# Kernel optimization log

Hardware: AMD Instinct MI355X
Metric: run time of the kernel (lower is better)

The kernel has to match this reference:

```python
import jax, jax.numpy as jnp
import numpy as np
import math

N_HEAD = 8
LN_EPS = 1e-5


def _layernorm(x, w, b):
    # Biased variance as in the triton kernel: var = E[x^2] - mean^2
    mean = jnp.mean(x, axis=-1, keepdims=True)
    var = jnp.mean(x * x, axis=-1, keepdims=True) - mean * mean
    return (x - mean) * jax.lax.rsqrt(var + LN_EPS) * w + b


def _gelu_tanh(x):
    # matches triton gelu: tanh approximation
    return 0.5 * x * (1.0 + jnp.tanh(0.7978845608 * (x + 0.044715 * x * x * x)))


def _causal_attention(qkv, n_head):
    B, T, C3 = qkv.shape
    C = C3 // 3
    D = C // n_head
    q, k, v = jnp.split(qkv, 3, axis=-1)
    q = q.reshape(B, T, n_head, D)
    k = k.reshape(B, T, n_head, D)
    v = v.reshape(B, T, n_head, D)
    scale = 1.0 / math.sqrt(D)
    scores = jnp.einsum('bqhd,bkhd->bhqk', q, k) * scale  # [B,H,T,T]
    causal = jnp.tril(jnp.ones((T, T), dtype=bool))
    scores = jnp.where(causal, scores, -jnp.inf)
    p = jax.nn.softmax(scores, axis=-1)
    out = jnp.einsum('bhqk,bkhd->bqhd', p, v)
    return out.reshape(B, T, C)


def setup_inputs() -> dict:
    key = jax.random.key(0)
    ks = jax.random.split(key, 8)
    B, T, C = 8, 2048, 768
    s = 0.02
    return {
        'x': jax.random.normal(ks[0], (B, T, C), jnp.float32),
        'ln1_w': jnp.ones((C,), jnp.float32),
        'ln1_b': jnp.zeros((C,), jnp.float32),
        'w_qkv': jax.random.normal(ks[1], (3 * C, C), jnp.float32) * s,
        'b_qkv': jnp.zeros((3 * C,), jnp.float32),
        'w_attn_proj': jax.random.normal(ks[2], (C, C), jnp.float32) * s,
        'b_attn_proj': jnp.zeros((C,), jnp.float32),
        'ln2_w': jnp.ones((C,), jnp.float32),
        'ln2_b': jnp.zeros((C,), jnp.float32),
        'w_fc': jax.random.normal(ks[3], (4 * C, C), jnp.float32) * s,
        'b_fc': jnp.zeros((4 * C,), jnp.float32),
        'w_mlp_proj': jax.random.normal(ks[4], (C, 4 * C), jnp.float32) * s,
        'b_mlp_proj': jnp.zeros((C,), jnp.float32),
    }


def reference(x, ln1_w, ln1_b, w_qkv, b_qkv, w_attn_proj, b_attn_proj,
              ln2_w, ln2_b, w_fc, b_fc, w_mlp_proj, b_mlp_proj):
    # attention block: fused LN + QKV linear, causal flash attention, out proj, residual
    qkv = _layernorm(x, ln1_w, ln1_b) @ w_qkv.T + b_qkv          # [B,T,3C]
    att = _causal_attention(qkv, N_HEAD)                          # [B,T,C]
    x = x + (att @ w_attn_proj.T + b_attn_proj)
    # MLP block: fused LN + fc + gelu, proj, residual
    h = _gelu_tanh(_layernorm(x, ln2_w, ln2_b) @ w_fc.T + b_fc)   # [B,T,4C]
    x = x + (h @ w_mlp_proj.T + b_mlp_proj)
    return x
```

## Files before the change

### kernel.cpp

```cpp
#include <hip/hip_runtime.h>
#include <hip/hip_bf16.h>
#include <cstdint>
#include <cstddef>

typedef __attribute__((ext_vector_type(8))) short bf16x8;
typedef __attribute__((ext_vector_type(4))) short bf16x4;
typedef __attribute__((ext_vector_type(4))) float f32x4;
typedef __attribute__((ext_vector_type(16))) float f32x16;

#define GLB_AS(p) ((const __attribute__((address_space(1))) void*)(p))
#define LDS_AS(p) ((__attribute__((address_space(3))) void*)(p))

__device__ __forceinline__ short f2bf(float f) {
    union { float f; unsigned u; } x; x.f = f;
    unsigned r = (x.u + 0x7fffu + ((x.u >> 16) & 1u)) >> 16;
    return (short)r;
}
__device__ __forceinline__ unsigned packbf2(float a, float b) {
    union { float f; unsigned u; } x, y; x.f = a; y.f = b;
    return (x.u >> 16) | (y.u & 0xffff0000u);
}
__device__ __forceinline__ f32x4 MF(bf16x8 a, bf16x8 b, f32x4 c) {
    return __builtin_amdgcn_mfma_f32_16x16x32_bf16(a, b, c, 0, 0, 0);
}
__device__ __forceinline__ f32x16 MF32(bf16x8 a, bf16x8 b, f32x16 c) {
    return __builtin_amdgcn_mfma_f32_32x32x16_bf16(a, b, c, 0, 0, 0);
}

__global__ __launch_bounds__(256) void k_cast_bf16(const float* __restrict__ src,
                                                   short* __restrict__ dst, int n4) {
    int i = blockIdx.x * 256 + threadIdx.x;
    int stride = gridDim.x * 256;
    for (; i < n4; i += stride) {
        float4 v = ((const float4*)src)[i];
        bf16x4 o;
        o[0] = f2bf(v.x); o[1] = f2bf(v.y); o[2] = f2bf(v.z); o[3] = f2bf(v.w);
        ((bf16x4*)dst)[i] = o;
    }
}

__global__ __launch_bounds__(256) void k_layernorm(const float* __restrict__ x,
                                                   const float* __restrict__ w,
                                                   const float* __restrict__ b,
                                                   short* __restrict__ out) {
    const int row = blockIdx.x;
    const int tid = threadIdx.x;
    const float* xr = x + (size_t)row * 768;
    float v0 = xr[tid], v1 = xr[tid + 256], v2 = xr[tid + 512];
    float s = v0 + v1 + v2;
    float ss = v0 * v0 + v1 * v1 + v2 * v2;
    #pragma unroll
    for (int m = 32; m; m >>= 1) { s += __shfl_xor(s, m); ss += __shfl_xor(ss, m); }
    __shared__ float red[8];
    int wid = tid >> 6, lane = tid & 63;
    if (lane == 0) { red[wid] = s; red[4 + wid] = ss; }
    __syncthreads();
    s = red[0] + red[1] + red[2] + red[3];
    ss = red[4] + red[5] + red[6] + red[7];
    float mean = s * (1.f / 768.f);
    float var = ss * (1.f / 768.f) - mean * mean;
    float inv = rsqrtf(var + 1e-5f);
    short* orow = out + (size_t)row * 768;
    orow[tid]       = f2bf((v0 - mean) * inv * w[tid]       + b[tid]);
    orow[tid + 256] = f2bf((v1 - mean) * inv * w[tid + 256] + b[tid + 256]);
    orow[tid + 512] = f2bf((v2 - mean) * inv * w[tid + 512] + b[tid + 512]);
}

#define QUAD(MB, NB, AA, BB)                                                   \
    do {                                                                       \
        __builtin_amdgcn_s_setprio(1);                                         \
        _Pragma("unroll")                                                      \
        for (int mi = 0; mi < 4; ++mi)                                         \
            _Pragma("unroll")                                                  \
            for (int ni = 0; ni < 2; ++ni) {                                   \
                acc[(MB) + mi][(NB) + ni] =                                    \
                    MF(AA[mi][0], BB[ni][0], acc[(MB) + mi][(NB) + ni]);       \
                acc[(MB) + mi][(NB) + ni] =                                    \
                    MF(AA[mi][1], BB[ni][1], acc[(MB) + mi][(NB) + ni]);       \
            }                                                                  \
        __builtin_amdgcn_s_setprio(0);                                         \
    } while (0)

template <int EPI>
__global__ __launch_bounds__(512, 2) void k_gemm256(const short* __restrict__ A,
                                                    const short* __restrict__ B,
                                                    const float* __restrict__ bias,
                                                    const float* __restrict__ res,
                                                    void* __restrict__ out,
                                                    int M, int N, int K) {
    __shared__ short As3[3][256 * 64];
    __shared__ short Bs2[2][256 * 64];
    const int tid = threadIdx.x, lane = tid & 63, wid = tid >> 6;
    const int l4 = lane & 15, lh = lane >> 4;
    const int wm = wid >> 2, wn = wid & 3;
    const int gx = gridDim.x;
    const int nwg = gx * gridDim.y;
    int wg = blockIdx.y * gx + blockIdx.x;
    { const int q = nwg >> 3; wg = (wg & 7) * q + (wg >> 3); }
    const int row0 = (wg / gx) * 256, col0 = (wg % gx) * 256;

    auto stage = [&](const short* __restrict__ src, int base_row, short* lds,
                     int mh, int k0) {
        #pragma unroll
        for (int i = 0; i < 2; ++i) {
            const int chunk = wid * 2 + i;
            const int dl = mh * 16384 + chunk * 1024 + lane * 16;
            const int r = dl >> 7;
            const int cb = (dl & 127) ^ ((r & 7) << 4);
            __builtin_amdgcn_global_load_lds(
                GLB_AS(src + (size_t)(base_row + r) * K + k0 + (cb >> 1)),
                LDS_AS(lds + mh * 8192 + chunk * 512), 16, 0, 0);
        }
    };
    auto rd = [&](const short* lds, int r, int kb) -> bf16x8 {
        return *(const bf16x8*)((const char*)lds + r * 128 +
                                ((kb * 64 + lh * 16) ^ ((r & 7) << 4)));
    };

    f32x4 acc[8][4] = {};
    bf16x8 a[4][2], b0[2][2], b1[2][2];
    const int NT = K >> 6;

    stage(A, row0, As3[0], 0, 0);  stage(A, row0, As3[0], 1, 0);
    stage(B, col0, Bs2[0], 0, 0);  stage(B, col0, Bs2[0], 1, 0);
    stage(A, row0, As3[1], 0, 64); stage(A, row0, As3[1], 1, 64);
    asm volatile("s_waitcnt vmcnt(4)" ::: "memory");
    __builtin_amdgcn_s_barrier();

    int ia = 0, ia2 = 2, ib = 0;
    for (int t = 0; t < NT; ++t) {
        const short* Ac = As3[ia];
        const short* Bc = Bs2[ib];
        const int ib2 = ib ^ 1;
        #pragma unroll
        for (int mi = 0; mi < 4; ++mi) {
            const int r = wm * 128 + mi * 16 + l4;
            a[mi][0] = rd(Ac, r, 0); a[mi][1] = rd(Ac, r, 1);
        }
        #pragma unroll
        for (int ni = 0; ni < 2; ++ni) {
            const int r = wn * 64 + ni * 16 + l4;
            b0[ni][0] = rd(Bc, r, 0); b0[ni][1] = rd(Bc, r, 1);
        }
        if (t + 1 < NT) {
            const int kn = (t + 1) << 6;
            stage(B, col0, Bs2[ib2], 0, kn);
            stage(B, col0, Bs2[ib2], 1, kn);
        }
        if (t + 2 < NT) {
            const int kn2 = (t + 2) << 6;
            stage(A, row0, As3[ia2], 0, kn2);
            stage(A, row0, As3[ia2], 1, kn2);
        }
        QUAD(0, 0, a, b0);
        __builtin_amdgcn_s_barrier();
        #pragma unroll
        for (int ni = 0; ni < 2; ++ni) {
            const int r = wn * 64 + (2 + ni) * 16 + l4;
            b1[ni][0] = rd(Bc, r, 0); b1[ni][1] = rd(Bc, r, 1);
        }
        QUAD(0, 2, a, b1);
        __builtin_amdgcn_s_barrier();
        #pragma unroll
        for (int mi = 0; mi < 4; ++mi) {
            const int r = wm * 128 + (4 + mi) * 16 + l4;
            a[mi][0] = rd(Ac, r, 0); a[mi][1] = rd(Ac, r, 1);
        }
        QUAD(4, 2, a, b1);
        __builtin_amdgcn_s_barrier();
        QUAD(4, 0, a, b0);
        if (t + 2 < NT) {
            asm volatile("s_waitcnt vmcnt(4)" ::: "memory");
        } else if (t + 1 < NT) {
            asm volatile("s_waitcnt vmcnt(0)" ::: "memory");
        }
        __builtin_amdgcn_s_barrier();
        ia = (ia + 1 == 3) ? 0 : ia + 1;
        ia2 = (ia2 + 1 == 3) ? 0 : ia2 + 1;
        ib = ib2;
    }

    #pragma unroll
    for (int mi = 0; mi < 8; ++mi) {
        const int rowb = row0 + wm * 128 + mi * 16 + lh * 4;
        #pragma unroll
        for (int ni = 0; ni < 4; ++ni) {
            const int col = col0 + wn * 64 + ni * 16 + l4;
            const float bv = bias[col];
            #pragma unroll
            for (int j = 0; j < 4; ++j) {
                const size_t idx = (size_t)(rowb + j) * N + col;
                float v = acc[mi][ni][j] + bv;
                if (EPI == 0) {
                    ((short*)out)[idx] = f2bf(v);
                } else if (EPI == 1) {
                    ((float*)out)[idx] = v + res[idx];
                } else {
                    float u = v + 0.044715f * v * v * v;
                    float t = 1.f - 2.f / (__expf(1.5957691216f * u) + 1.f);
                    ((short*)out)[idx] = f2bf(0.5f * v * (1.f + t));
                }
            }
        }
    }
}

__global__ __launch_bounds__(256, 2) void k_attn6(const short* __restrict__ qkv,
                                                  short* __restrict__ att) {
    __shared__ short Ks[2][64 * 128];
    __shared__ short Vs[2][96 * 64];
    const int tid = threadIdx.x, lane = tid & 63, wid = tid >> 6;
    const int lq = lane & 31, hi = lane >> 5;
    const int h = blockIdx.y, b = blockIdx.z;
    const short* base = qkv + (size_t)b * 2048 * 2304 + h * 96;
    const short* Kb = base + 768;
    const short* Vb = base + 1536;
    const int vkvr = (tid / 12) * 4, vd0 = (tid % 12) * 8;
    const int vslot = (vkvr & ~12) | ((vkvr & 4) << 1) | ((vkvr & 8) >> 1);
    bf16x8 vreg[4];
    const float QSC = 0.14724445f;

    auto stageK = [&](int jt, int bb) {
        const int kv0 = jt * 64;
        for (int c = wid; c < 16; c += 4) {
            const int dl = c * 1024 + lane * 16;
            const int row = dl >> 8;
            const int scol = (dl & 255) ^ ((row & 7) << 4);
            __builtin_amdgcn_global_load_lds(GLB_AS(Kb + (size_t)(kv0 + row) * 2304 + (scol >> 1)),
                                             LDS_AS(&Ks[bb][c * 512]), 16, 0, 0);
        }
    };
    auto loadV = [&](int jt) {
        if (tid < 192) {
            const int kv0 = jt * 64;
            #pragma unroll
            for (int e = 0; e < 4; ++e)
                vreg[e] = *(const bf16x8*)(Vb + (size_t)(kv0 + vkvr + e) * 2304 + vd0);
        }
    };
    auto writeV = [&](int bb) {
        if (tid < 192) {
            #pragma unroll
            for (int f = 0; f < 8; ++f) {
                const int row = vd0 + f;
                const int sw = ((row & 7) ^ ((row >> 3) & 7)) << 4;
                const int byte = (row * 128 + vslot * 2) ^ sw;
                bf16x4 w4;
                w4[0] = vreg[0][f]; w4[1] = vreg[1][f]; w4[2] = vreg[2][f]; w4[3] = vreg[3][f];
                *(bf16x4*)((char*)&Vs[bb][0] + byte) = w4;
            }
        }
    };

    for (int half = 0; half < 2; ++half) {
        const int qt = half ? 15 - (int)blockIdx.x : (int)blockIdx.x;
        const int q0 = qt * 128 + wid * 32;
        const int qa = q0 + lq;

        bf16x8 qf[6];
        #pragma unroll
        for (int kb = 0; kb < 6; ++kb) {
            bf16x8 v = *(const bf16x8*)(base + (size_t)qa * 2304 + kb * 16 + hi * 8);
            #pragma unroll
            for (int e = 0; e < 8; ++e) {
                union { unsigned u; float f; } x;
                x.u = ((unsigned)(unsigned short)v[e]) << 16;
                qf[kb][e] = f2bf(x.f * QSC);
            }
        }

        f32x16 o[3] = {};
        float lrow = 0.f;
        const int nt = 2 * qt + 2;

        stageK(0, 0);
        loadV(0);
        asm volatile("s_waitcnt vmcnt(0)" ::: "memory");
        writeV(0);
        __syncthreads();

        int cur = 0;
        for (int jt = 0; jt < nt; ++jt) {
            const int nxt = cur ^ 1;
            const bool more = (jt + 1 < nt);
            if (more) { stageK(jt + 1, nxt); loadV(jt + 1); }

            const int kv0 = jt * 64;
            if (kv0 <= q0 + 31) {
                const bool full = (kv0 + 63 <= q0);
                f32x16 s0 = {}, s1 = {};
                #pragma unroll
                for (int kb = 0; kb < 6; ++kb) {
                    const int r0 = lq, r1 = 32 + lq;
                    bf16x8 kf0 = *(const bf16x8*)((const char*)&Ks[cur][0] +
                                  r0 * 256 + ((kb * 32 + hi * 16) ^ ((r0 & 7) << 4)));
                    bf16x8 kf1 = *(const bf16x8*)((const char*)&Ks[cur][0] +
                                  r1 * 256 + ((kb * 32 + hi * 16) ^ ((r1 & 7) << 4)));
                    s0 = MF32(kf0, qf[kb], s0);
                    s1 = MF32(kf1, qf[kb], s1);
                }
                if (!full) {
                    #pragma unroll
                    for (int r = 0; r < 16; ++r) {
                        const int kvl = (r & 3) + 8 * (r >> 2) + 4 * hi;
                        if (kv0 + kvl > qa) s0[r] = -INFINITY;
                        if (kv0 + 32 + kvl > qa) s1[r] = -INFINITY;
                    }
                }
                #pragma unroll
                for (int r = 0; r < 16; ++r) {
                    s0[r] = exp2f(s0[r]);
                    s1[r] = exp2f(s1[r]);
                }
                float ar[16];
                #pragma unroll
                for (int r = 0; r < 16; ++r) ar[r] = s0[r] + s1[r];
                #pragma unroll
                for (int st = 8; st; st >>= 1)
                    #pragma unroll
                    for (int r = 0; r < 8; ++r)
                        if (r < st) ar[r] += ar[r + st];
                lrow += ar[0] + __shfl_xor(ar[0], 32);
                unsigned pk0[8], pk1[8];
                #pragma unroll
                for (int j = 0; j < 8; ++j) {
                    pk0[j] = packbf2(s0[2 * j], s0[2 * j + 1]);
                    pk1[j] = packbf2(s1[2 * j], s1[2 * j + 1]);
                }
                #pragma unroll
                for (int db = 0; db < 3; ++db) {
                    const int vrow = db * 32 + lq;
                    const int vsw = ((vrow & 7) ^ ((vrow >> 3) & 7)) << 4;
                    #pragma unroll
                    for (int c = 0; c < 4; ++c) {
                        bf16x8 vf = *(const bf16x8*)((const char*)&Vs[cur][0] +
                                     vrow * 128 + ((c * 32 + hi * 16) ^ vsw));
                        union { unsigned u[4]; bf16x8 v; } pa;
                        const unsigned* pk = (c < 2) ? pk0 : pk1;
                        const int o4 = (c & 1) * 4;
                        pa.u[0] = pk[o4]; pa.u[1] = pk[o4 + 1];
                        pa.u[2] = pk[o4 + 2]; pa.u[3] = pk[o4 + 3];
                        o[db] = MF32(vf, pa.v, o[db]);
                    }
                }
            }

            if (more) {
                asm volatile("s_waitcnt vmcnt(0)" ::: "memory");
                writeV(nxt);
            }
            __syncthreads();
            cur = nxt;
        }

        const float inv = 1.f / lrow;
        short* orow = att + (size_t)((size_t)b * 2048 + qa) * 768 + h * 96;
        #pragma unroll
        for (int db = 0; db < 3; ++db)
            #pragma unroll
            for (int j = 0; j < 4; ++j) {
                bf16x4 ov;
                #pragma unroll
                for (int e = 0; e < 4; ++e) ov[e] = f2bf(o[db][4 * j + e] * inv);
                *(bf16x4*)(orow + db * 32 + 8 * j + 4 * hi) = ov;
            }
    }
}

extern "C" void kernel_launch(void* const* d_in, const int* in_sizes, int n_in,
                              void* d_out, int out_size, void* d_ws, size_t ws_size,
                              hipStream_t stream) {
    (void)in_sizes; (void)n_in; (void)out_size; (void)ws_size;
    const float* x      = (const float*)d_in[0];
    const float* ln1_w  = (const float*)d_in[1];
    const float* ln1_b  = (const float*)d_in[2];
    const float* w_qkv  = (const float*)d_in[3];
    const float* b_qkv  = (const float*)d_in[4];
    const float* w_proj = (const float*)d_in[5];
    const float* b_proj = (const float*)d_in[6];
    const float* ln2_w  = (const float*)d_in[7];
    const float* ln2_b  = (const float*)d_in[8];
    const float* w_fc   = (const float*)d_in[9];
    const float* b_fc   = (const float*)d_in[10];
    const float* w_mlp  = (const float*)d_in[11];
    const float* b_mlp  = (const float*)d_in[12];

    const int C = 768, M = 8 * 2048;

    char* ws = (char*)d_ws;
    size_t off = 0;
    auto alloc = [&](size_t bytes) {
        char* p = ws + off;
        off += (bytes + 255) & ~(size_t)255;
        return p;
    };
    short* wqkv_b = (short*)alloc((size_t)3 * C * C * 2);
    short* wproj_b = (short*)alloc((size_t)C * C * 2);
    short* wfc_b  = (short*)alloc((size_t)4 * C * C * 2);
    short* wmlp_b = (short*)alloc((size_t)4 * C * C * 2);
    short* bufA   = (short*)alloc((size_t)M * C * 2);
    short* bufB   = (short*)alloc((size_t)M * 4 * C * 2);
    float* x2     = (float*)alloc((size_t)M * C * 4);

    k_cast_bf16<<<dim3(432), dim3(256), 0, stream>>>(w_qkv, wqkv_b, 3 * C * C / 4);
    k_cast_bf16<<<dim3(144), dim3(256), 0, stream>>>(w_proj, wproj_b, C * C / 4);
    k_cast_bf16<<<dim3(576), dim3(256), 0, stream>>>(w_fc, wfc_b, 4 * C * C / 4);
    k_cast_bf16<<<dim3(576), dim3(256), 0, stream>>>(w_mlp, wmlp_b, 4 * C * C / 4);

    k_layernorm<<<dim3(M), dim3(256), 0, stream>>>(x, ln1_w, ln1_b, bufA);
    k_gemm256<0><<<dim3(2304 / 256, M / 256), dim3(512), 0, stream>>>(
        bufA, wqkv_b, b_qkv, nullptr, bufB, M, 2304, C);
    k_attn6<<<dim3(8, 8, 8), dim3(256), 0, stream>>>(bufB, bufA);
    k_gemm256<1><<<dim3(C / 256, M / 256), dim3(512), 0, stream>>>(
        bufA, wproj_b, b_proj, x, x2, M, C, C);
    k_layernorm<<<dim3(M), dim3(256), 0, stream>>>(x2, ln2_w, ln2_b, bufA);
    k_gemm256<2><<<dim3(3072 / 256, M / 256), dim3(512), 0, stream>>>(
        bufA, wfc_b, b_fc, nullptr, bufB, M, 3072, C);
    k_gemm256<1><<<dim3(C / 256, M / 256), dim3(512), 0, stream>>>(
        bufB, wmlp_b, b_mlp, x2, d_out, M, C, 4 * C);
}
```

Baseline: 478.0 us.

## Template GEMM N-tile width, simplify to double buffering, fuse weight casts

```diff
diff --git a/kernel.cpp b/kernel.cpp
--- a/kernel.cpp
+++ b/kernel.cpp
@@ -27,15 +27,35 @@
     return __builtin_amdgcn_mfma_f32_32x32x16_bf16(a, b, c, 0, 0, 0);
 }
 
-__global__ __launch_bounds__(256) void k_cast_bf16(const float* __restrict__ src,
-                                                   short* __restrict__ dst, int n4) {
+__global__ __launch_bounds__(256) void k_cast4(const float* __restrict__ s0,
+                                               const float* __restrict__ s1,
+                                               const float* __restrict__ s2,
+                                               const float* __restrict__ s3,
+                                               short* __restrict__ d0,
+                                               short* __restrict__ d1,
+                                               short* __restrict__ d2,
+                                               short* __restrict__ d3,
+                                               int n0, int n1, int n2, int n3) {
+    const int total = n0 + n1 + n2 + n3;
     int i = blockIdx.x * 256 + threadIdx.x;
-    int stride = gridDim.x * 256;
-    for (; i < n4; i += stride) {
-        float4 v = ((const float4*)src)[i];
+    const int stride = gridDim.x * 256;
+    for (; i < total; i += stride) {
+        int j = i;
+        const float* s; short* d;
+        if (j < n0) { s = s0; d = d0; }
+        else {
+            j -= n0;
+            if (j < n1) { s = s1; d = d1; }
+            else {
+                j -= n1;
+                if (j < n2) { s = s2; d = d2; }
+                else { j -= n2; s = s3; d = d3; }
+            }
+        }
+        float4 v = ((const float4*)s)[j];
         bf16x4 o;
         o[0] = f2bf(v.x); o[1] = f2bf(v.y); o[2] = f2bf(v.z); o[3] = f2bf(v.w);
-        ((bf16x4*)dst)[i] = o;
+        ((bf16x4*)d)[j] = o;
     }
 }
 
@@ -66,30 +86,15 @@
     orow[tid + 512] = f2bf((v2 - mean) * inv * w[tid + 512] + b[tid + 512]);
 }
 
-#define QUAD(MB, NB, AA, BB)                                                   \
-    do {                                                                       \
-        __builtin_amdgcn_s_setprio(1);                                         \
-        _Pragma("unroll")                                                      \
-        for (int mi = 0; mi < 4; ++mi)                                         \
-            _Pragma("unroll")                                                  \
-            for (int ni = 0; ni < 2; ++ni) {                                   \
-                acc[(MB) + mi][(NB) + ni] =                                    \
-                    MF(AA[mi][0], BB[ni][0], acc[(MB) + mi][(NB) + ni]);       \
-                acc[(MB) + mi][(NB) + ni] =                                    \
-                    MF(AA[mi][1], BB[ni][1], acc[(MB) + mi][(NB) + ni]);       \
-            }                                                                  \
-        __builtin_amdgcn_s_setprio(0);                                         \
-    } while (0)
-
-template <int EPI>
+template <int EPI, int NFR>
 __global__ __launch_bounds__(512, 2) void k_gemm256(const short* __restrict__ A,
                                                     const short* __restrict__ B,
                                                     const float* __restrict__ bias,
                                                     const float* __restrict__ res,
                                                     void* __restrict__ out,
                                                     int M, int N, int K) {
-    __shared__ short As3[3][256 * 64];
-    __shared__ short Bs2[2][256 * 64];
+    __shared__ short As2[2][256 * 64];
+    __shared__ short Bs2[2][NFR * 64 * 64];
     const int tid = threadIdx.x, lane = tid & 63, wid = tid >> 6;
     const int l4 = lane & 15, lh = lane >> 4;
     const int wm = wid >> 2, wn = wid & 3;
@@ -97,10 +102,9 @@
     const int nwg = gx * gridDim.y;
     int wg = blockIdx.y * gx + blockIdx.x;
     { const int q = nwg >> 3; wg = (wg & 7) * q + (wg >> 3); }
-    const int row0 = (wg / gx) * 256, col0 = (wg % gx) * 256;
-
-    auto stage = [&](const short* __restrict__ src, int base_row, short* lds,
-                     int mh, int k0) {
+    const int row0 = (wg / gx) * 256, col0 = (wg % gx) * (NFR * 64);
+
+    auto stageA = [&](short* lds, int mh, int k0) {
         #pragma unroll
         for (int i = 0; i < 2; ++i) {
             const int chunk = wid * 2 + i;
@@ -108,8 +112,20 @@
             const int r = dl >> 7;
             const int cb = (dl & 127) ^ ((r & 7) << 4);
             __builtin_amdgcn_global_load_lds(
-                GLB_AS(src + (size_t)(base_row + r) * K + k0 + (cb >> 1)),
+                GLB_AS(A + (size_t)(row0 + r) * K + k0 + (cb >> 1)),
                 LDS_AS(lds + mh * 8192 + chunk * 512), 16, 0, 0);
+        }
+    };
+    auto stageB = [&](short* lds, int k0) {
+        #pragma unroll
+        for (int i = 0; i < NFR; ++i) {
+            const int chunk = wid * NFR + i;
+            const int dl = chunk * 1024 + lane * 16;
+            const int r = dl >> 7;
+            const int cb = (dl & 127) ^ ((r & 7) << 4);
+            __builtin_amdgcn_global_load_lds(
+                GLB_AS(B + (size_t)(col0 + r) * K + k0 + (cb >> 1)),
+                LDS_AS(lds + chunk * 512), 16, 0, 0);
         }
     };
     auto rd = [&](const short* lds, int r, int kb) -> bf16x8 {
@@ -117,21 +133,22 @@
                                 ((kb * 64 + lh * 16) ^ ((r & 7) << 4)));
     };
 
-    f32x4 acc[8][4] = {};
+    f32x4 acc[8][NFR] = {};
     bf16x8 a[4][2], b0[2][2], b1[2][2];
     const int NT = K >> 6;
 
-    stage(A, row0, As3[0], 0, 0);  stage(A, row0, As3[0], 1, 0);
-    stage(B, col0, Bs2[0], 0, 0);  stage(B, col0, Bs2[0], 1, 0);
-    stage(A, row0, As3[1], 0, 64); stage(A, row0, As3[1], 1, 64);
-    asm volatile("s_waitcnt vmcnt(4)" ::: "memory");
+    stageA(As2[0], 0, 0);
+    stageA(As2[0], 1, 0);
+    stageB(Bs2[0], 0);
+    asm volatile("s_waitcnt vmcnt(0)" ::: "memory");
     __builtin_amdgcn_s_barrier();
 
-    int ia = 0, ia2 = 2, ib = 0;
     for (int t = 0; t < NT; ++t) {
-        const short* Ac = As3[ia];
-        const short* Bc = Bs2[ib];
-        const int ib2 = ib ^ 1;
+        const int cur = t & 1, nxt = cur ^ 1;
+        const short* Ac = As2[cur];
+        const short* Bc = Bs2[cur];
+        const int kn = (t + 1) << 6;
+        const bool more = (t + 1 < NT);
         #pragma unroll
         for (int mi = 0; mi < 4; ++mi) {
             const int r = wm * 128 + mi * 16 + l4;
@@ -139,53 +156,70 @@
         }
         #pragma unroll
         for (int ni = 0; ni < 2; ++ni) {
-            const int r = wn * 64 + ni * 16 + l4;
+            const int r = wn * (NFR * 16) + ni * 16 + l4;
             b0[ni][0] = rd(Bc, r, 0); b0[ni][1] = rd(Bc, r, 1);
         }
-        if (t + 1 < NT) {
-            const int kn = (t + 1) << 6;
-            stage(B, col0, Bs2[ib2], 0, kn);
-            stage(B, col0, Bs2[ib2], 1, kn);
-        }
-        if (t + 2 < NT) {
-            const int kn2 = (t + 2) << 6;
-            stage(A, row0, As3[ia2], 0, kn2);
-            stage(A, row0, As3[ia2], 1, kn2);
-        }
-        QUAD(0, 0, a, b0);
+        if (more) { stageA(As2[nxt], 0, kn); stageA(As2[nxt], 1, kn); }
+        __builtin_amdgcn_s_setprio(1);
+        #pragma unroll
+        for (int mi = 0; mi < 4; ++mi)
+            #pragma unroll
+            for (int ni = 0; ni < 2; ++ni) {
+                acc[mi][ni] = MF(a[mi][0], b0[ni][0], acc[mi][ni]);
+                acc[mi][ni] = MF(a[mi][1], b0[ni][1], acc[mi][ni]);
+            }
+        __builtin_amdgcn_s_setprio(0);
         __builtin_amdgcn_s_barrier();
         #pragma unroll
-        for (int ni = 0; ni < 2; ++ni) {
-            const int r = wn * 64 + (2 + ni) * 16 + l4;
-            b1[ni][0] = rd(Bc, r, 0); b1[ni][1] = rd(Bc, r, 1);
-        }
-        QUAD(0, 2, a, b1);
+        for (int j = 0; j < NFR - 2; ++j) {
+            const int r = wn * (NFR * 16) + (2 + j) * 16 + l4;
+            b1[j][0] = rd(Bc, r, 0); b1[j][1] = rd(Bc, r, 1);
+        }
+        if (more) stageB(Bs2[nxt], kn);
+        __builtin_amdgcn_s_setprio(1);
+        #pragma unroll
+        for (int mi = 0; mi < 4; ++mi)
+            #pragma unroll
+            for (int j = 0; j < NFR - 2; ++j) {
+                acc[mi][2 + j] = MF(a[mi][0], b1[j][0], acc[mi][2 + j]);
+                acc[mi][2 + j] = MF(a[mi][1], b1[j][1], acc[mi][2 + j]);
+            }
+        __builtin_amdgcn_s_setprio(0);
         __builtin_amdgcn_s_barrier();
         #pragma unroll
         for (int mi = 0; mi < 4; ++mi) {
             const int r = wm * 128 + (4 + mi) * 16 + l4;
             a[mi][0] = rd(Ac, r, 0); a[mi][1] = rd(Ac, r, 1);
         }
-        QUAD(4, 2, a, b1);
+        __builtin_amdgcn_s_setprio(1);
+        #pragma unroll
+        for (int mi = 0; mi < 4; ++mi)
+            #pragma unroll
+            for (int j = 0; j < NFR - 2; ++j) {
+                acc[4 + mi][2 + j] = MF(a[mi][0], b1[j][0], acc[4 + mi][2 + j]);
+                acc[4 + mi][2 + j] = MF(a[mi][1], b1[j][1], acc[4 + mi][2 + j]);
+            }
+        __builtin_amdgcn_s_setprio(0);
         __builtin_amdgcn_s_barrier();
-        QUAD(4, 0, a, b0);
-        if (t + 2 < NT) {
-            asm volatile("s_waitcnt vmcnt(4)" ::: "memory");
-        } else if (t + 1 < NT) {
-            asm volatile("s_waitcnt vmcnt(0)" ::: "memory");
-        }
+        __builtin_amdgcn_s_setprio(1);
+        #pragma unroll
+        for (int mi = 0; mi < 4; ++mi)
+            #pragma unroll
+            for (int ni = 0; ni < 2; ++ni) {
+                acc[4 + mi][ni] = MF(a[mi][0], b0[ni][0], acc[4 + mi][ni]);
+                acc[4 + mi][ni] = MF(a[mi][1], b0[ni][1], acc[4 + mi][ni]);
+            }
+        __builtin_amdgcn_s_setprio(0);
+        asm volatile("s_waitcnt vmcnt(0)" ::: "memory");
         __builtin_amdgcn_s_barrier();
-        ia = (ia + 1 == 3) ? 0 : ia + 1;
-        ia2 = (ia2 + 1 == 3) ? 0 : ia2 + 1;
-        ib = ib2;
     }
 
     #pragma unroll
     for (int mi = 0; mi < 8; ++mi) {
         const int rowb = row0 + wm * 128 + mi * 16 + lh * 4;
         #pragma unroll
-        for (int ni = 0; ni < 4; ++ni) {
-            const int col = col0 + wn * 64 + ni * 16 + l4;
+        for (int ni = 0; ni < NFR; ++ni) {
+            const int col = col0 + wn * (NFR * 16) + ni * 16 + l4;
             const float bv = bias[col];
             #pragma unroll
             for (int j = 0; j < 4; ++j) {
@@ -402,20 +436,19 @@
     short* bufB   = (short*)alloc((size_t)M * 4 * C * 2);
     float* x2     = (float*)alloc((size_t)M * C * 4);
 
-    k_cast_bf16<<<dim3(432), dim3(256), 0, stream>>>(w_qkv, wqkv_b, 3 * C * C / 4);
-    k_cast_bf16<<<dim3(144), dim3(256), 0, stream>>>(w_proj, wproj_b, C * C / 4);
-    k_cast_bf16<<<dim3(576), dim3(256), 0, stream>>>(w_fc, wfc_b, 4 * C * C / 4);
-    k_cast_bf16<<<dim3(576), dim3(256), 0, stream>>>(w_mlp, wmlp_b, 4 * C * C / 4);
+    k_cast4<<<dim3(1728), dim3(256), 0, stream>>>(
+        w_qkv, w_proj, w_fc, w_mlp, wqkv_b, wproj_b, wfc_b, wmlp_b,
+        3 * C * C / 4, C * C / 4, 4 * C * C / 4, 4 * C * C / 4);
 
     k_layernorm<<<dim3(M), dim3(256), 0, stream>>>(x, ln1_w, ln1_b, bufA);
-    k_gemm256<0><<<dim3(2304 / 256, M / 256), dim3(512), 0, stream>>>(
+    k_gemm256<0, 3><<<dim3(2304 / 192, M / 256), dim3(512), 0, stream>>>(
         bufA, wqkv_b, b_qkv, nullptr, bufB, M, 2304, C);
     k_attn6<<<dim3(8, 8, 8), dim3(256), 0, stream>>>(bufB, bufA);
-    k_gemm256<1><<<dim3(C / 256, M / 256), dim3(512), 0, stream>>>(
+    k_gemm256<1, 3><<<dim3(768 / 192, M / 256), dim3(512), 0, stream>>>(
         bufA, wproj_b, b_proj, x, x2, M, C, C);
     k_layernorm<<<dim3(M), dim3(256), 0, stream>>>(x2, ln2_w, ln2_b, bufA);
-    k_gemm256<2><<<dim3(3072 / 256, M / 256), dim3(512), 0, stream>>>(
+    k_gemm256<2, 4><<<dim3(3072 / 256, M / 256), dim3(512), 0, stream>>>(
         bufA, wfc_b, b_fc, nullptr, bufB, M, 3072, C);
-    k_gemm256<1><<<dim3(C / 256, M / 256), dim3(512), 0, stream>>>(
+    k_gemm256<1, 3><<<dim3(768 / 192, M / 256), dim3(512), 0, stream>>>(
         bufB, wmlp_b, b_mlp, x2, d_out, M, C, 4 * C);
 }
```

After: 434.8 us. 1.1x faster.
